# Optimization experiments

Hardware: AMD Instinct MI355X
Metric: run time of the kernel (lower is better)

## Reference

```python
import jax, jax.numpy as jnp
import numpy as np

N_NODES = 100000
N_EDGES = 300000
N_TYPES = 3
HID = 128
EMB = 64
N_GRAPHS = 4096
T_STEPS = 4


def setup_inputs() -> dict:
    key = jax.random.key(0)
    ks = jax.random.split(key, 12)
    s = 1.0 / np.sqrt(HID)
    return {
        "node_features": jax.random.normal(ks[0], (N_NODES, HID), jnp.float32),
        "edge_index": jax.random.randint(ks[1], (N_TYPES, 2, N_EDGES), 0, N_NODES),
        "node_to_graph_id": jnp.sort(jax.random.randint(ks[2], (N_NODES,), 0, N_GRAPHS)),
        "W_msg": jax.random.normal(ks[3], (N_TYPES, HID, HID), jnp.float32) * s,
        "b_msg": jnp.zeros((N_TYPES, HID), jnp.float32),
        "W_ih": jax.random.normal(ks[4], (3 * HID, HID), jnp.float32) * s,
        "W_hh": jax.random.normal(ks[5], (3 * HID, HID), jnp.float32) * s,
        "b_ih": jnp.zeros((3 * HID,), jnp.float32),
        "b_hh": jnp.zeros((3 * HID,), jnp.float32),
        "W_proj": jax.random.normal(ks[6], (EMB, HID), jnp.float32) * s,
        "b_proj": jnp.zeros((EMB,), jnp.float32),
        "W_gate": jax.random.normal(ks[7], (EMB, HID), jnp.float32) * s,
        "b_gate": jnp.zeros((EMB,), jnp.float32),
    }


def _gru_cell(m, h, W_ih, W_hh, b_ih, b_hh):
    # torch.nn.GRUCell math; gates ordered (r, z, n)
    gi = m @ W_ih.T + b_ih          # [N, 3H]
    gh = h @ W_hh.T + b_hh          # [N, 3H]
    i_r, i_z, i_n = jnp.split(gi, 3, axis=-1)
    h_r, h_z, h_n = jnp.split(gh, 3, axis=-1)
    r = jax.nn.sigmoid(i_r + h_r)
    z = jax.nn.sigmoid(i_z + h_z)
    n = jnp.tanh(i_n + r * h_n)
    return (1.0 - z) * n + z * h


def reference(node_features, edge_index, node_to_graph_id,
              W_msg, b_msg, W_ih, W_hh, b_ih, b_hh,
              W_proj, b_proj, W_gate, b_gate):
    h = node_features  # [N, H]

    def per_type(eidx, W, b, h):
        src, dst = eidx[0], eidx[1]
        m = h[src] @ W + b  # gather + per-edge-type linear, [E, H]
        return jax.ops.segment_sum(m, dst, num_segments=N_NODES)

    for _ in range(T_STEPS):  # fixed small T: python loop is fine
        msgs = jax.vmap(per_type, in_axes=(0, 0, 0, None))(edge_index, W_msg, b_msg, h)
        m = msgs.sum(axis=0)  # [N, H] aggregated over edge types
        h = _gru_cell(m, h, W_ih, W_hh, b_ih, b_hh)

    # gated index_add graph readout (mlp_down is identity)
    proj = h @ W_proj.T + b_proj                 # [N, E]
    gate = jax.nn.sigmoid(h @ W_gate.T + b_gate)  # [N, E]
    graph_feats = jax.ops.segment_sum(gate * proj, node_to_graph_id,
                                      num_segments=N_GRAPHS)
    return graph_feats
```

## Files before the change

kernel.cpp:

```cpp
#include <hip/hip_runtime.h>
#include <hip/hip_bf16.h>
#include <math.h>

#define NN 100000
#define NNP 100096
#define NE 300000
#define HID 128
#define EMB 64
#define NG 4096
#define DEG_CAP 32
#define XS 512

typedef __bf16 bf16x8 __attribute__((ext_vector_type(8)));
typedef float  f32x16 __attribute__((ext_vector_type(16)));
typedef short  short8 __attribute__((ext_vector_type(8)));

typedef const __attribute__((address_space(1))) unsigned int* gas_u32;
typedef __attribute__((address_space(3))) unsigned int* las_u32;

__device__ __forceinline__ void gload16(const void* g, void* l) {
    __builtin_amdgcn_global_load_lds((gas_u32)g, (las_u32)l, 16, 0, 0);
}

__device__ __forceinline__ float bf2f(unsigned short u) {
    unsigned int x = ((unsigned int)u) << 16;
    return __builtin_bit_cast(float, x);
}
__device__ __forceinline__ unsigned short f2bf(float f) {
    unsigned int x = __builtin_bit_cast(unsigned int, f);
    unsigned int r = x + 0x7fff + ((x >> 16) & 1);
    return (unsigned short)(r >> 16);
}
__device__ __forceinline__ float sigm(float x) { return 1.f / (1.f + __expf(-x)); }

#define MFMA(A, B, C) __builtin_amdgcn_mfma_f32_32x32x16_bf16( \
    __builtin_bit_cast(bf16x8, A), __builtin_bit_cast(bf16x8, B), C, 0, 0, 0)

__global__ __launch_bounds__(256) void k_init(const float* __restrict__ nf,
                                              unsigned short* __restrict__ Y) {
    int id = blockIdx.x * 256 + threadIdx.x;
    int n = id >> 7, c = id & 127;
    Y[(long)n * HID + c] = (n < NN) ? f2bf(nf[(long)n * HID + c]) : (unsigned short)0;
}

__global__ __launch_bounds__(256) void k_build_csr(const int* __restrict__ ei,
                                                   int* __restrict__ deg,
                                                   int* __restrict__ csr) {
    int id = blockIdx.x * 256 + threadIdx.x;
    if (id >= 3 * NE) return;
    int t = id / NE;
    int i = id - t * NE;
    int src = ei[(t * 2 + 0) * NE + i];
    int dst = ei[(t * 2 + 1) * NE + i];
    int p = atomicAdd(&deg[t * NN + dst], 1);
    if (p < DEG_CAP) csr[((long)t * NN + dst) * DEG_CAP + p] = src;
}

__global__ __launch_bounds__(256) void k_pack_deg(const int* __restrict__ deg,
                                                  int4* __restrict__ degp) {
    int n = blockIdx.x * 256 + threadIdx.x;
    if (n >= NNP) return;
    int4 v; v.x = 0; v.y = 0; v.z = 0; v.w = 0;
    if (n < NN) { v.x = deg[n]; v.y = deg[NN + n]; v.z = deg[2 * NN + n]; }
    degp[n] = v;
}

__global__ __launch_bounds__(512) void k_build_w(const float* __restrict__ Wmsg,
                                                 const float* __restrict__ Wih,
                                                 const float* __restrict__ Whh,
                                                 unsigned short* __restrict__ Bf) {
    int np = blockIdx.x;
    int k = threadIdx.x;
    int c = np >> 2, sec = np & 3;
    float v = 0.f;
    if (k < 384) {
        if (sec < 3) {
            int t = k >> 7, kk = k & 127;
            const float* wm = Wmsg + ((long)t * HID + kk) * HID;
            const float* wi = Wih + (long)(sec * HID + c) * HID;
            float s = 0.f;
            for (int j = 0; j < HID; j++) s += wm[j] * wi[j];
            v = s;
        }
    } else {
        int kk = k - 384;
        if (sec == 0)      v = Whh[(long)c * HID + kk];
        else if (sec == 1) v = Whh[(long)(HID + c) * HID + kk];
        else if (sec == 3) v = Whh[(long)(2 * HID + c) * HID + kk];
    }
    int nb = np >> 5, nl = np & 31;
    int k16 = k >> 4, kgg = (k >> 3) & 1, e = k & 7;
    Bf[((((nb * 32 + k16) * 2 + kgg) * 32 + nl) << 3) + e] = f2bf(v);
}

__global__ __launch_bounds__(512) void k_build_bias(const float* __restrict__ bih,
                                                    const float* __restrict__ bhh,
                                                    const float* __restrict__ bmsg,
                                                    const float* __restrict__ Wih,
                                                    float* __restrict__ bbig,
                                                    float* __restrict__ Bdeg) {
    int np = threadIdx.x;
    int c = np >> 2, sec = np & 3;
    float b;
    if (sec == 0)      b = bih[c] + bhh[c];
    else if (sec == 1) b = bih[HID + c] + bhh[HID + c];
    else if (sec == 2) b = bih[2 * HID + c];
    else               b = bhh[2 * HID + c];
    bbig[np] = b;
    for (int t = 0; t < 3; t++) {
        float s = 0.f;
        if (sec < 3) {
            const float* wi = Wih + (long)(sec * HID + c) * HID;
            const float* bm = bmsg + t * HID;
            for (int j = 0; j < HID; j++) s += bm[j] * wi[j];
        }
        Bdeg[t * 512 + np] = s;
    }
}

__global__ __launch_bounds__(256) void k_agg(const unsigned short* __restrict__ Y,
                                             unsigned short* __restrict__ X,
                                             const int* __restrict__ deg,
                                             const int* __restrict__ csr) {
    const int lane = threadIdx.x & 63;
    const long n = (long)blockIdx.x * 4 + (threadIdx.x >> 6);
    const int g = lane >> 4;
    const int c16 = lane & 15;
    const int l31 = lane & 31;

    int d[3], il[3];
#pragma unroll
    for (int t = 0; t < 3; t++) {
        int dt = deg[t * NN + n];
        d[t] = dt > DEG_CAP ? DEG_CAP : dt;
        il[t] = csr[((long)t * NN + n) * DEG_CAP + l31];
    }
#pragma unroll
    for (int t = 0; t < 3; t++) {
        float acc[8] = {0.f, 0.f, 0.f, 0.f, 0.f, 0.f, 0.f, 0.f};
        int rounds = (d[t] + 3) >> 2;
        for (int r = 0; r < rounds; r++) {
            int j = r * 4 + g;
            int idx = __shfl(il[t], j & 31);
            if (j < d[t]) {
                short8 v = *(const short8*)(Y + (long)idx * HID + c16 * 8);
#pragma unroll
                for (int q = 0; q < 8; q++) acc[q] += bf2f((unsigned short)v[q]);
            }
        }
#pragma unroll
        for (int q = 0; q < 8; q++) {
            acc[q] += __shfl_xor(acc[q], 16);
            acc[q] += __shfl_xor(acc[q], 32);
        }
        if (g == 0) {
            short8 o;
#pragma unroll
            for (int q = 0; q < 8; q++) o[q] = (short)f2bf(acc[q]);
            *(short8*)(X + n * XS + t * HID + c16 * 8) = o;
        }
    }
    if (g == 1) {
        short8 v = *(const short8*)(Y + n * HID + c16 * 8);
        *(short8*)(X + n * XS + 384 + c16 * 8) = v;
    }
}

__global__ __launch_bounds__(512, 4) void k_gru_mfma(
        const unsigned short* __restrict__ X,
        const unsigned short* __restrict__ Y,
        unsigned short* __restrict__ Yw,
        const unsigned short* __restrict__ Bf,
        const float* __restrict__ bbig, const float* __restrict__ Bdeg,
        const int4* __restrict__ degp) {
    __shared__ char lds[66048];

    const int tid = threadIdx.x;
    const int lane = tid & 63;
    const int wv = tid >> 6;
    const int r31 = lane & 31;
    const int kg = lane >> 5;
    const long row0 = (long)blockIdx.x * 64;

    f32x16 acc[2][2];
#pragma unroll
    for (int i = 0; i < 2; i++)
#pragma unroll
        for (int j = 0; j < 2; j++) acc[i][j] = (f32x16)(0.0f);

    const char* pAl = (const char*)X + (row0 + r31) * 1024 + kg * 16;
#define STAGE_A(HALF)                                                           \
    {                                                                           \
        _Pragma("unroll")                                                       \
        for (int jj = 0; jj < 4; jj++) {                                        \
            const int f = wv * 4 + jj;                                          \
            gload16(pAl + (f & 1) * 32768 + ((HALF) * 16 + (f >> 1)) * 32,      \
                    lds + f * 1024);                                            \
        }                                                                       \
    }

    const unsigned short* pB0 = Bf + (wv * 2 + 0) * 16384 + lane * 8;
    const unsigned short* pB1 = Bf + (wv * 2 + 1) * 16384 + lane * 8;

    STAGE_A(0);
    __syncthreads();

#pragma unroll
    for (int k16l = 0; k16l < 16; k16l++) {
        short8 a0 = *(const short8*)(lds + (k16l * 2 + 0) * 1024 + lane * 16);
        short8 a1 = *(const short8*)(lds + (k16l * 2 + 1) * 1024 + lane * 16);
        short8 b0 = *(const short8*)(pB0 + k16l * 512);
        short8 b1 = *(const short8*)(pB1 + k16l * 512);
        acc[0][0] = MFMA(a0, b0, acc[0][0]);
        acc[0][1] = MFMA(a0, b1, acc[0][1]);
        acc[1][0] = MFMA(a1, b0, acc[1][0]);
        acc[1][1] = MFMA(a1, b1, acc[1][1]);
    }

    __syncthreads();
    STAGE_A(1);
    __syncthreads();

#pragma unroll
    for (int k16l = 0; k16l < 16; k16l++) {
        const int k16g = 16 + k16l;
        short8 a0 = *(const short8*)(lds + (k16l * 2 + 0) * 1024 + lane * 16);
        short8 a1 = *(const short8*)(lds + (k16l * 2 + 1) * 1024 + lane * 16);
        short8 b0 = *(const short8*)(pB0 + k16g * 512);
        short8 b1 = *(const short8*)(pB1 + k16g * 512);
        acc[0][0] = MFMA(a0, b0, acc[0][0]);
        acc[0][1] = MFMA(a0, b1, acc[0][1]);
        acc[1][0] = MFMA(a1, b0, acc[1][0]);
        acc[1][1] = MFMA(a1, b1, acc[1][1]);
    }

    float* EX = (float*)lds;
    const int ch = tid & 127;
    const int r5b = tid >> 7;
    const float4 bb = *(const float4*)(bbig + ch * 4);
    const float4 q0v = *(const float4*)(Bdeg + ch * 4);
    const float4 q1v = *(const float4*)(Bdeg + 512 + ch * 4);
    const float4 q2v = *(const float4*)(Bdeg + 1024 + ch * 4);

#pragma unroll
    for (int half = 0; half < 2; half++) {
        __syncthreads();
#pragma unroll
        for (int ct = 0; ct < 2; ct++) {
            const int col = wv * 64 + ct * 32 + r31;
#pragma unroll
            for (int reg = 0; reg < 16; reg++) {
                int r5 = (reg & 3) + 8 * (reg >> 2) + 4 * kg;
                EX[r5 * 516 + col] = half ? acc[1][ct][reg] : acc[0][ct][reg];
            }
        }
        __syncthreads();
#pragma unroll
        for (int i = 0; i < 8; i++) {
            const int r5 = r5b + 4 * i;
            long grow = row0 + half * 32 + r5;
            int4 dg = degp[grow];
            float dgx = (float)dg.x, dgy = (float)dg.y, dgz = (float)dg.z;
            float4 v = *(const float4*)(EX + r5 * 516 + ch * 4);
            float Sr = v.x + bb.x + dgx * q0v.x + dgy * q1v.x + dgz * q2v.x;
            float Sz = v.y + bb.y + dgx * q0v.y + dgy * q1v.y + dgz * q2v.y;
            float In = v.z + bb.z + dgx * q0v.z + dgy * q1v.z + dgz * q2v.z;
            float Hn = v.w + bb.w;
            float rr = sigm(Sr);
            float zz = sigm(Sz);
            float tt = In + rr * Hn;
            float ee = __expf(2.f * tt);
            float nn = 1.f - 2.f / (ee + 1.f);
            float hv = (1.f - zz) * nn + zz * bf2f(Y[grow * HID + ch]);
            Yw[grow * HID + ch] = f2bf(hv);
        }
    }
}

__global__ __launch_bounds__(256) void k_readout(const unsigned short* __restrict__ Y,
                                                 const int* __restrict__ n2g,
                                                 const float* __restrict__ Wp,
                                                 const float* __restrict__ bp,
                                                 const float* __restrict__ Wg,
                                                 const float* __restrict__ bg,
                                                 float* __restrict__ out) {
    __shared__ float hs[32][132];
    __shared__ float Ws[64][129];
    int tid = threadIdx.x;
    long row0 = (long)blockIdx.x * 32;
    int rg = tid >> 5, cg = tid & 31;
    float acc[4][4];
#pragma unroll
    for (int r = 0; r < 4; r++)
#pragma unroll
        for (int c = 0; c < 4; c++) acc[r][c] = 0.f;

#pragma unroll
    for (int p = 0; p < 2; p++) {
        int e = p * 256 + tid;
        int r = e >> 4, c8 = e & 15;
        short8 v = *(const short8*)(Y + (row0 + r) * HID + c8 * 8);
#pragma unroll
        for (int j = 0; j < 8; j++) hs[r][c8 * 8 + j] = bf2f((unsigned short)v[j]);
    }
    for (int kc = 0; kc < 128; kc += 64) {
        __syncthreads();
#pragma unroll
        for (int p = 0; p < 8; p++) {
            int idx = p * 256 + tid;
            int j = idx >> 4, q = idx & 15;
            const float* Wsrc = (j < 64) ? Wp : Wg;
            float4 w = *(const float4*)&Wsrc[(j & 63) * HID + kc + q * 4];
            Ws[q * 4 + 0][j] = w.x;
            Ws[q * 4 + 1][j] = w.y;
            Ws[q * 4 + 2][j] = w.z;
            Ws[q * 4 + 3][j] = w.w;
        }
        __syncthreads();
#pragma unroll 8
        for (int k = 0; k < 64; k++) {
            float a[4], w[4];
#pragma unroll
            for (int r = 0; r < 4; r++) a[r] = hs[rg * 4 + r][kc + k];
#pragma unroll
            for (int c = 0; c < 4; c++) w[c] = Ws[k][cg + 32 * c];
#pragma unroll
            for (int r = 0; r < 4; r++)
#pragma unroll
                for (int c = 0; c < 4; c++) acc[r][c] += a[r] * w[c];
        }
    }
#pragma unroll
    for (int r = 0; r < 4; r++) {
        long row = row0 + rg * 4 + r;
        if (row < NN) {
            int g = n2g[row];
            float pv0 = acc[r][0] + bp[cg];
            float pv1 = acc[r][1] + bp[cg + 32];
            float gv0 = acc[r][2] + bg[cg];
            float gv1 = acc[r][3] + bg[cg + 32];
            atomicAdd(&out[g * EMB + cg],      pv0 * sigm(gv0));
            atomicAdd(&out[g * EMB + cg + 32], pv1 * sigm(gv1));
        }
    }
}

extern "C" void kernel_launch(void* const* d_in, const int* in_sizes, int n_in,
                              void* d_out, int out_size, void* d_ws, size_t ws_size,
                              hipStream_t stream) {
    const float* node_features = (const float*)d_in[0];
    const int*   edge_index    = (const int*)d_in[1];
    const int*   n2g           = (const int*)d_in[2];
    const float* W_msg         = (const float*)d_in[3];
    const float* b_msg         = (const float*)d_in[4];
    const float* W_ih          = (const float*)d_in[5];
    const float* W_hh          = (const float*)d_in[6];
    const float* b_ih          = (const float*)d_in[7];
    const float* b_hh          = (const float*)d_in[8];
    const float* W_proj        = (const float*)d_in[9];
    const float* b_proj        = (const float*)d_in[10];
    const float* W_gate        = (const float*)d_in[11];
    const float* b_gate        = (const float*)d_in[12];

    char* ws = (char*)d_ws;
    unsigned short* X    = (unsigned short*)(ws);
    unsigned short* Y    = (unsigned short*)(ws + 102498304);
    unsigned short* Bf   = (unsigned short*)(ws + 128122880);
    float*          bbig = (float*)         (ws + 128647168);
    float*          Bdeg = (float*)         (ws + 128649216);
    int4*           degp = (int4*)          (ws + 128655360);
    int*            deg  = (int*)           (ws + 130256896);
    int*            csr  = (int*)           (ws + 131456896);

    float* out = (float*)d_out;

    hipMemsetAsync(out, 0, (size_t)NG * EMB * sizeof(float), stream);
    hipMemsetAsync(deg, 0, (size_t)3 * NN * sizeof(int), stream);

    k_init<<<dim3((NNP * HID) / 256), dim3(256), 0, stream>>>(node_features, Y);
    k_build_csr<<<dim3((3 * NE + 255) / 256), dim3(256), 0, stream>>>(edge_index, deg, csr);
    k_pack_deg<<<dim3(NNP / 256), dim3(256), 0, stream>>>(deg, degp);
    k_build_w<<<dim3(512), dim3(512), 0, stream>>>(W_msg, W_ih, W_hh, Bf);
    k_build_bias<<<dim3(1), dim3(512), 0, stream>>>(b_ih, b_hh, b_msg, W_ih, bbig, Bdeg);

    for (int step = 0; step < 4; step++) {
        k_agg<<<dim3(NN / 4), dim3(256), 0, stream>>>(Y, X, deg, csr);
        k_gru_mfma<<<dim3(NNP / 64), dim3(512), 0, stream>>>(X, Y, Y, Bf,
                                                             bbig, Bdeg, degp);
    }
    k_readout<<<dim3(NN / 32), dim3(256), 0, stream>>>(Y, n2g, W_proj, b_proj,
                                                       W_gate, b_gate, out);
}
```

Before: 854.0 us.

## Fuse neighbor aggregation into GRU MFMA kernel with ping-pong hidden buffers

Merges the gather/segment-sum kernel into the GRU MFMA kernel. Each block aggregates neighbor rows for its 64 nodes straight into LDS in the MFMA A-tile layout, so the 512-wide intermediate X buffer is never written to or read from global memory. The hidden state now alternates between two buffers across steps, which avoids read/write races. The cost is lower gather parallelism per node: each 16-lane group walks its edge list serially, and there is one block per 64 rows with the MFMA work waiting behind the gather phase.

```diff
diff --git a/kernel.cpp b/kernel.cpp
--- a/kernel.cpp
+++ b/kernel.cpp
@@ -9,18 +9,10 @@
 #define EMB 64
 #define NG 4096
 #define DEG_CAP 32
-#define XS 512
 
 typedef __bf16 bf16x8 __attribute__((ext_vector_type(8)));
 typedef float  f32x16 __attribute__((ext_vector_type(16)));
 typedef short  short8 __attribute__((ext_vector_type(8)));
-
-typedef const __attribute__((address_space(1))) unsigned int* gas_u32;
-typedef __attribute__((address_space(3))) unsigned int* las_u32;
-
-__device__ __forceinline__ void gload16(const void* g, void* l) {
-    __builtin_amdgcn_global_load_lds((gas_u32)g, (las_u32)l, 16, 0, 0);
-}
 
 __device__ __forceinline__ float bf2f(unsigned short u) {
     unsigned int x = ((unsigned int)u) << 16;
@@ -118,116 +110,73 @@
     }
 }
 
-__global__ __launch_bounds__(256) void k_agg(const unsigned short* __restrict__ Y,
-                                             unsigned short* __restrict__ X,
-                                             const int* __restrict__ deg,
-                                             const int* __restrict__ csr) {
-    const int lane = threadIdx.x & 63;
-    const long n = (long)blockIdx.x * 4 + (threadIdx.x >> 6);
-    const int g = lane >> 4;
-    const int c16 = lane & 15;
-    const int l31 = lane & 31;
-
-    int d[3], il[3];
-#pragma unroll
-    for (int t = 0; t < 3; t++) {
-        int dt = deg[t * NN + n];
-        d[t] = dt > DEG_CAP ? DEG_CAP : dt;
-        il[t] = csr[((long)t * NN + n) * DEG_CAP + l31];
-    }
-#pragma unroll
-    for (int t = 0; t < 3; t++) {
-        float acc[8] = {0.f, 0.f, 0.f, 0.f, 0.f, 0.f, 0.f, 0.f};
-        int rounds = (d[t] + 3) >> 2;
-        for (int r = 0; r < rounds; r++) {
-            int j = r * 4 + g;
-            int idx = __shfl(il[t], j & 31);
-            if (j < d[t]) {
-                short8 v = *(const short8*)(Y + (long)idx * HID + c16 * 8);
-#pragma unroll
-                for (int q = 0; q < 8; q++) acc[q] += bf2f((unsigned short)v[q]);
-            }
-        }
-#pragma unroll
-        for (int q = 0; q < 8; q++) {
-            acc[q] += __shfl_xor(acc[q], 16);
-            acc[q] += __shfl_xor(acc[q], 32);
-        }
-        if (g == 0) {
-            short8 o;
-#pragma unroll
-            for (int q = 0; q < 8; q++) o[q] = (short)f2bf(acc[q]);
-            *(short8*)(X + n * XS + t * HID + c16 * 8) = o;
-        }
-    }
-    if (g == 1) {
-        short8 v = *(const short8*)(Y + n * HID + c16 * 8);
-        *(short8*)(X + n * XS + 384 + c16 * 8) = v;
-    }
-}
-
-__global__ __launch_bounds__(512, 4) void k_gru_mfma(
-        const unsigned short* __restrict__ X,
-        const unsigned short* __restrict__ Y,
-        unsigned short* __restrict__ Yw,
+__global__ __launch_bounds__(512, 4) void k_step(
+        const unsigned short* __restrict__ Yin,
+        unsigned short* __restrict__ Yout,
         const unsigned short* __restrict__ Bf,
         const float* __restrict__ bbig, const float* __restrict__ Bdeg,
-        const int4* __restrict__ degp) {
+        const int4* __restrict__ degp,
+        const int* __restrict__ deg,
+        const int* __restrict__ csr) {
     __shared__ char lds[66048];
 
     const int tid = threadIdx.x;
     const int lane = tid & 63;
     const int wv = tid >> 6;
+    const int sec = lane >> 4;
+    const int c16 = lane & 15;
+    const long row0 = (long)blockIdx.x * 64;
+
+#pragma unroll
+    for (int i = 0; i < 8; i++) {
+        const int rloc = wv * 8 + i;
+        const long n = row0 + rloc;
+        int d = 0, il0 = 0, il1 = 0;
+        if (sec < 3 && n < NN) {
+            d = deg[sec * NN + n];
+            if (d > DEG_CAP) d = DEG_CAP;
+            const long cb = ((long)sec * NN + n) * DEG_CAP;
+            il0 = csr[cb + c16];
+            il1 = csr[cb + 16 + c16];
+        }
+        float ac[8] = {0.f, 0.f, 0.f, 0.f, 0.f, 0.f, 0.f, 0.f};
+#pragma unroll 2
+        for (int j = 0; j < d; j++) {
+            int idx = __shfl((j < 16) ? il0 : il1, (lane & 48) + (j & 15));
+            short8 v = *(const short8*)(Yin + (long)idx * HID + c16 * 8);
+#pragma unroll
+            for (int q = 0; q < 8; q++) ac[q] += bf2f((unsigned short)v[q]);
+        }
+        short8 o;
+        if (sec == 3) {
+            o = *(const short8*)(Yin + n * HID + c16 * 8);
+        } else {
+#pragma unroll
+            for (int q = 0; q < 8; q++) o[q] = (short)f2bf(ac[q]);
+        }
+        const int k16 = sec * 8 + (c16 >> 1);
+        const int f = k16 * 2 + (rloc >> 5);
+        *(short8*)(lds + f * 1024 + (((c16 & 1) << 5) + (rloc & 31)) * 16) = o;
+    }
+
     const int r31 = lane & 31;
-    const int kg = lane >> 5;
-    const long row0 = (long)blockIdx.x * 64;
-
-    f32x16 acc[2][2];
-#pragma unroll
-    for (int i = 0; i < 2; i++)
-#pragma unroll
-        for (int j = 0; j < 2; j++) acc[i][j] = (f32x16)(0.0f);
-
-    const char* pAl = (const char*)X + (row0 + r31) * 1024 + kg * 16;
-#define STAGE_A(HALF)                                                           \
-    {                                                                           \
-        _Pragma("unroll")                                                       \
-        for (int jj = 0; jj < 4; jj++) {                                        \
-            const int f = wv * 4 + jj;                                          \
-            gload16(pAl + (f & 1) * 32768 + ((HALF) * 16 + (f >> 1)) * 32,      \
-                    lds + f * 1024);                                            \
-        }                                                                       \
-    }
-
     const unsigned short* pB0 = Bf + (wv * 2 + 0) * 16384 + lane * 8;
     const unsigned short* pB1 = Bf + (wv * 2 + 1) * 16384 + lane * 8;
 
-    STAGE_A(0);
+    f32x16 acc[2][2];
+#pragma unroll
+    for (int i = 0; i < 2; i++)
+#pragma unroll
+        for (int j = 0; j < 2; j++) acc[i][j] = (f32x16)(0.0f);
+
     __syncthreads();
 
 #pragma unroll
-    for (int k16l = 0; k16l < 16; k16l++) {
-        short8 a0 = *(const short8*)(lds + (k16l * 2 + 0) * 1024 + lane * 16);
-        short8 a1 = *(const short8*)(lds + (k16l * 2 + 1) * 1024 + lane * 16);
-        short8 b0 = *(const short8*)(pB0 + k16l * 512);
-        short8 b1 = *(const short8*)(pB1 + k16l * 512);
-        acc[0][0] = MFMA(a0, b0, acc[0][0]);
-        acc[0][1] = MFMA(a0, b1, acc[0][1]);
-        acc[1][0] = MFMA(a1, b0, acc[1][0]);
-        acc[1][1] = MFMA(a1, b1, acc[1][1]);
-    }
-
-    __syncthreads();
-    STAGE_A(1);
-    __syncthreads();
-
-#pragma unroll
-    for (int k16l = 0; k16l < 16; k16l++) {
-        const int k16g = 16 + k16l;
-        short8 a0 = *(const short8*)(lds + (k16l * 2 + 0) * 1024 + lane * 16);
-        short8 a1 = *(const short8*)(lds + (k16l * 2 + 1) * 1024 + lane * 16);
-        short8 b0 = *(const short8*)(pB0 + k16g * 512);
-        short8 b1 = *(const short8*)(pB1 + k16g * 512);
+    for (int k16 = 0; k16 < 32; k16++) {
+        short8 a0 = *(const short8*)(lds + (k16 * 2 + 0) * 1024 + lane * 16);
+        short8 a1 = *(const short8*)(lds + (k16 * 2 + 1) * 1024 + lane * 16);
+        short8 b0 = *(const short8*)(pB0 + k16 * 512);
+        short8 b1 = *(const short8*)(pB1 + k16 * 512);
         acc[0][0] = MFMA(a0, b0, acc[0][0]);
         acc[0][1] = MFMA(a0, b1, acc[0][1]);
         acc[1][0] = MFMA(a1, b0, acc[1][0]);
@@ -241,6 +190,7 @@
     const float4 q0v = *(const float4*)(Bdeg + ch * 4);
     const float4 q1v = *(const float4*)(Bdeg + 512 + ch * 4);
     const float4 q2v = *(const float4*)(Bdeg + 1024 + ch * 4);
+    const int kg = lane >> 5;
 
 #pragma unroll
     for (int half = 0; half < 2; half++) {
@@ -271,8 +221,8 @@
             float tt = In + rr * Hn;
             float ee = __expf(2.f * tt);
             float nn = 1.f - 2.f / (ee + 1.f);
-            float hv = (1.f - zz) * nn + zz * bf2f(Y[grow * HID + ch]);
-            Yw[grow * HID + ch] = f2bf(hv);
+            float hv = (1.f - zz) * nn + zz * bf2f(Yin[grow * HID + ch]);
+            Yout[grow * HID + ch] = f2bf(hv);
         }
     }
 }
@@ -363,31 +313,31 @@
     const float* b_gate        = (const float*)d_in[12];
 
     char* ws = (char*)d_ws;
-    unsigned short* X    = (unsigned short*)(ws);
-    unsigned short* Y    = (unsigned short*)(ws + 102498304);
-    unsigned short* Bf   = (unsigned short*)(ws + 128122880);
-    float*          bbig = (float*)         (ws + 128647168);
-    float*          Bdeg = (float*)         (ws + 128649216);
-    int4*           degp = (int4*)          (ws + 128655360);
-    int*            deg  = (int*)           (ws + 130256896);
-    int*            csr  = (int*)           (ws + 131456896);
+    unsigned short* Y0   = (unsigned short*)(ws);
+    unsigned short* Y1   = (unsigned short*)(ws + 25624576);
+    unsigned short* Bf   = (unsigned short*)(ws + 51249152);
+    float*          bbig = (float*)         (ws + 51773440);
+    float*          Bdeg = (float*)         (ws + 51775488);
+    int4*           degp = (int4*)          (ws + 51781632);
+    int*            deg  = (int*)           (ws + 53383168);
+    int*            csr  = (int*)           (ws + 54583168);
 
     float* out = (float*)d_out;
 
     hipMemsetAsync(out, 0, (size_t)NG * EMB * sizeof(float), stream);
     hipMemsetAsync(deg, 0, (size_t)3 * NN * sizeof(int), stream);
 
-    k_init<<<dim3((NNP * HID) / 256), dim3(256), 0, stream>>>(node_features, Y);
+    k_init<<<dim3((NNP * HID) / 256), dim3(256), 0, stream>>>(node_features, Y0);
     k_build_csr<<<dim3((3 * NE + 255) / 256), dim3(256), 0, stream>>>(edge_index, deg, csr);
     k_pack_deg<<<dim3(NNP / 256), dim3(256), 0, stream>>>(deg, degp);
     k_build_w<<<dim3(512), dim3(512), 0, stream>>>(W_msg, W_ih, W_hh, Bf);
     k_build_bias<<<dim3(1), dim3(512), 0, stream>>>(b_ih, b_hh, b_msg, W_ih, bbig, Bdeg);
 
-    for (int step = 0; step < 4; step++) {
-        k_agg<<<dim3(NN / 4), dim3(256), 0, stream>>>(Y, X, deg, csr);
-        k_gru_mfma<<<dim3(NNP / 64), dim3(512), 0, stream>>>(X, Y, Y, Bf,
-                                                             bbig, Bdeg, degp);
-    }
-    k_readout<<<dim3(NN / 32), dim3(256), 0, stream>>>(Y, n2g, W_proj, b_proj,
+    k_step<<<dim3(NNP / 64), dim3(512), 0, stream>>>(Y0, Y1, Bf, bbig, Bdeg, degp, deg, csr);
+    k_step<<<dim3(NNP / 64), dim3(512), 0, stream>>>(Y1, Y0, Bf, bbig, Bdeg, degp, deg, csr);
+    k_step<<<dim3(NNP / 64), dim3(512), 0, stream>>>(Y0, Y1, Bf, bbig, Bdeg, degp, deg, csr);
+    k_step<<<dim3(NNP / 64), dim3(512), 0, stream>>>(Y1, Y0, Bf, bbig, Bdeg, degp, deg, csr);
+
+    k_readout<<<dim3(NN / 32), dim3(256), 0, stream>>>(Y0, n2g, W_proj, b_proj,
                                                        W_gate, b_gate, out);
 }
```

Result: slower. 874.1 us (+2.4%).

## Double GRU GEMM row tile, stage all A into LDS, prefetch B

Applied to the files above, without the earlier changes.

The GRU MFMA kernel now handles 128 rows per block instead of 64, with four accumulator row groups, so each B fragment loaded from global memory is reused across twice as many rows. Both K-halves of A are staged into 128 KB of dynamic LDS up front, so the second half loads while the first half computes and the mid-kernel barrier/restage is gone. B fragments are software-prefetched one K-step ahead in registers. The cost is one resident block per CU (launch bounds lowered to 2), more accumulator registers, and a dependence on large dynamic LDS being allowed at launch.

```diff
diff --git a/kernel.cpp b/kernel.cpp
--- a/kernel.cpp
+++ b/kernel.cpp
@@ -166,37 +166,37 @@
     }
 }
 
-__global__ __launch_bounds__(512, 4) void k_gru_mfma(
+__global__ __launch_bounds__(512, 2) void k_gru_mfma(
         const unsigned short* __restrict__ X,
         const unsigned short* __restrict__ Y,
         unsigned short* __restrict__ Yw,
         const unsigned short* __restrict__ Bf,
         const float* __restrict__ bbig, const float* __restrict__ Bdeg,
         const int4* __restrict__ degp) {
-    __shared__ char lds[66048];
+    extern __shared__ char lds[];
 
     const int tid = threadIdx.x;
     const int lane = tid & 63;
     const int wv = tid >> 6;
     const int r31 = lane & 31;
     const int kg = lane >> 5;
-    const long row0 = (long)blockIdx.x * 64;
-
-    f32x16 acc[2][2];
-#pragma unroll
-    for (int i = 0; i < 2; i++)
+    const long row0 = (long)blockIdx.x * 128;
+
+    f32x16 acc[4][2];
+#pragma unroll
+    for (int i = 0; i < 4; i++)
 #pragma unroll
         for (int j = 0; j < 2; j++) acc[i][j] = (f32x16)(0.0f);
 
-    const char* pAl = (const char*)X + (row0 + r31) * 1024 + kg * 16;
-#define STAGE_A(HALF)                                                           \
-    {                                                                           \
-        _Pragma("unroll")                                                       \
-        for (int jj = 0; jj < 4; jj++) {                                        \
-            const int f = wv * 4 + jj;                                          \
-            gload16(pAl + (f & 1) * 32768 + ((HALF) * 16 + (f >> 1)) * 32,      \
-                    lds + f * 1024);                                            \
-        }                                                                       \
+    const char* base = (const char*)X + (row0 + r31) * 1024 + kg * 16;
+#define STAGE_A(H)                                                            \
+    {                                                                         \
+        _Pragma("unroll")                                                     \
+        for (int jj = 0; jj < 8; jj++) {                                      \
+            const int f = wv * 8 + jj;                                        \
+            gload16(base + (long)(f & 3) * 32768 + ((H) * 16 + (f >> 2)) * 32,\
+                    lds + ((H) * 64 + f) * 1024);                             \
+        }                                                                     \
     }
 
     const unsigned short* pB0 = Bf + (wv * 2 + 0) * 16384 + lane * 8;
@@ -204,46 +204,69 @@
 
     STAGE_A(0);
     __syncthreads();
-
-#pragma unroll
-    for (int k16l = 0; k16l < 16; k16l++) {
-        short8 a0 = *(const short8*)(lds + (k16l * 2 + 0) * 1024 + lane * 16);
-        short8 a1 = *(const short8*)(lds + (k16l * 2 + 1) * 1024 + lane * 16);
-        short8 b0 = *(const short8*)(pB0 + k16l * 512);
-        short8 b1 = *(const short8*)(pB1 + k16l * 512);
-        acc[0][0] = MFMA(a0, b0, acc[0][0]);
-        acc[0][1] = MFMA(a0, b1, acc[0][1]);
-        acc[1][0] = MFMA(a1, b0, acc[1][0]);
-        acc[1][1] = MFMA(a1, b1, acc[1][1]);
-    }
-
+    STAGE_A(1);
+#undef STAGE_A
+
+    short8 pe0 = *(const short8*)(pB0);
+    short8 pe1 = *(const short8*)(pB1);
+    short8 po0 = *(const short8*)(pB0 + 512);
+    short8 po1 = *(const short8*)(pB1 + 512);
+
+#define KSTEP(K16, B0, B1)                                                    \
+    {                                                                         \
+        const char* fb = lds + (((K16) >> 4) * 64 + ((K16) & 15) * 4) * 1024  \
+                         + lane * 16;                                         \
+        short8 a0 = *(const short8*)(fb);                                     \
+        short8 a1 = *(const short8*)(fb + 1024);                              \
+        short8 a2 = *(const short8*)(fb + 2048);                              \
+        short8 a3 = *(const short8*)(fb + 3072);                              \
+        acc[0][0] = MFMA(a0, B0, acc[0][0]);                                  \
+        acc[0][1] = MFMA(a0, B1, acc[0][1]);                                  \
+        acc[1][0] = MFMA(a1, B0, acc[1][0]);                                  \
+        acc[1][1] = MFMA(a1, B1, acc[1][1]);                                  \
+        acc[2][0] = MFMA(a2, B0, acc[2][0]);                                  \
+        acc[2][1] = MFMA(a2, B1, acc[2][1]);                                  \
+        acc[3][0] = MFMA(a3, B0, acc[3][0]);                                  \
+        acc[3][1] = MFMA(a3, B1, acc[3][1]);                                  \
+    }
+
+#pragma unroll
+    for (int it = 0; it < 8; it++) {
+        const int k0 = 2 * it;
+        KSTEP(k0, pe0, pe1);
+        pe0 = *(const short8*)(pB0 + (k0 + 2) * 512);
+        pe1 = *(const short8*)(pB1 + (k0 + 2) * 512);
+        KSTEP(k0 + 1, po0, po1);
+        po0 = *(const short8*)(pB0 + (k0 + 3) * 512);
+        po1 = *(const short8*)(pB1 + (k0 + 3) * 512);
+    }
     __syncthreads();
-    STAGE_A(1);
-    __syncthreads();
-
-#pragma unroll
-    for (int k16l = 0; k16l < 16; k16l++) {
-        const int k16g = 16 + k16l;
-        short8 a0 = *(const short8*)(lds + (k16l * 2 + 0) * 1024 + lane * 16);
-        short8 a1 = *(const short8*)(lds + (k16l * 2 + 1) * 1024 + lane * 16);
-        short8 b0 = *(const short8*)(pB0 + k16g * 512);
-        short8 b1 = *(const short8*)(pB1 + k16g * 512);
-        acc[0][0] = MFMA(a0, b0, acc[0][0]);
-        acc[0][1] = MFMA(a0, b1, acc[0][1]);
-        acc[1][0] = MFMA(a1, b0, acc[1][0]);
-        acc[1][1] = MFMA(a1, b1, acc[1][1]);
-    }
+#pragma unroll
+    for (int it = 8; it < 16; it++) {
+        const int k0 = 2 * it;
+        KSTEP(k0, pe0, pe1);
+        if (it < 15) {
+            pe0 = *(const short8*)(pB0 + (k0 + 2) * 512);
+            pe1 = *(const short8*)(pB1 + (k0 + 2) * 512);
+        }
+        KSTEP(k0 + 1, po0, po1);
+        if (it < 15) {
+            po0 = *(const short8*)(pB0 + (k0 + 3) * 512);
+            po1 = *(const short8*)(pB1 + (k0 + 3) * 512);
+        }
+    }
+#undef KSTEP
 
     float* EX = (float*)lds;
     const int ch = tid & 127;
     const int r5b = tid >> 7;
-    const float4 bb = *(const float4*)(bbig + ch * 4);
+    const float4 bb  = *(const float4*)(bbig + ch * 4);
     const float4 q0v = *(const float4*)(Bdeg + ch * 4);
     const float4 q1v = *(const float4*)(Bdeg + 512 + ch * 4);
     const float4 q2v = *(const float4*)(Bdeg + 1024 + ch * 4);
 
 #pragma unroll
-    for (int half = 0; half < 2; half++) {
+    for (int q = 0; q < 4; q++) {
         __syncthreads();
 #pragma unroll
         for (int ct = 0; ct < 2; ct++) {
@@ -251,14 +274,14 @@
 #pragma unroll
             for (int reg = 0; reg < 16; reg++) {
                 int r5 = (reg & 3) + 8 * (reg >> 2) + 4 * kg;
-                EX[r5 * 516 + col] = half ? acc[1][ct][reg] : acc[0][ct][reg];
+                EX[r5 * 516 + col] = acc[q][ct][reg];
             }
         }
         __syncthreads();
 #pragma unroll
         for (int i = 0; i < 8; i++) {
             const int r5 = r5b + 4 * i;
-            long grow = row0 + half * 32 + r5;
+            long grow = row0 + q * 32 + r5;
             int4 dg = degp[grow];
             float dgx = (float)dg.x, dgy = (float)dg.y, dgz = (float)dg.z;
             float4 v = *(const float4*)(EX + r5 * 516 + ch * 4);
@@ -385,8 +408,8 @@
 
     for (int step = 0; step < 4; step++) {
         k_agg<<<dim3(NN / 4), dim3(256), 0, stream>>>(Y, X, deg, csr);
-        k_gru_mfma<<<dim3(NNP / 64), dim3(512), 0, stream>>>(X, Y, Y, Bf,
-                                                             bbig, Bdeg, degp);
+        k_gru_mfma<<<dim3(NNP / 128), dim3(512), 131072, stream>>>(X, Y, Y, Bf,
+                                                                   bbig, Bdeg, degp);
     }
     k_readout<<<dim3(NN / 32), dim3(256), 0, stream>>>(Y, n2g, W_proj, b_proj,
                                                        W_gate, b_gate, out);
```

New measurement: 953.9 us. 1.12x slower.

## Retile GRU MFMA kernel into 128x256 blocks with double-buffered LDS staging

Applied to the files above, without the earlier changes.

The GRU GEMM now uses a 2D grid. Each block computes 128 rows by 256 output columns, with the 8 waves laid out 2x4. Both the A tile and the B weight tile are streamed into LDS through global_load_lds in 16 k-steps, using a ping-pong double buffer so the next stage loads while the current one computes. Previously each block did all columns for 64 rows and read B directly from global memory. The epilogue is split into 16-row chunks with a smaller LDS footprint. The intent is to raise weight reuse and hide load latency, at the cost of more barriers and each block reading the A rows twice.

```diff
diff --git a/kernel.cpp b/kernel.cpp
--- a/kernel.cpp
+++ b/kernel.cpp
@@ -173,14 +173,17 @@
         const unsigned short* __restrict__ Bf,
         const float* __restrict__ bbig, const float* __restrict__ Bdeg,
         const int4* __restrict__ degp) {
-    __shared__ char lds[66048];
+    __shared__ char lds[49152];
 
     const int tid = threadIdx.x;
     const int lane = tid & 63;
     const int wv = tid >> 6;
+    const int wr = wv >> 2;
+    const int wc = wv & 3;
     const int r31 = lane & 31;
     const int kg = lane >> 5;
-    const long row0 = (long)blockIdx.x * 64;
+    const int bn = blockIdx.x;
+    const long row0 = (long)blockIdx.y * 128;
 
     f32x16 acc[2][2];
 #pragma unroll
@@ -188,91 +191,87 @@
 #pragma unroll
         for (int j = 0; j < 2; j++) acc[i][j] = (f32x16)(0.0f);
 
-    const char* pAl = (const char*)X + (row0 + r31) * 1024 + kg * 16;
-#define STAGE_A(HALF)                                                           \
-    {                                                                           \
-        _Pragma("unroll")                                                       \
-        for (int jj = 0; jj < 4; jj++) {                                        \
-            const int f = wv * 4 + jj;                                          \
-            gload16(pAl + (f & 1) * 32768 + ((HALF) * 16 + (f >> 1)) * 32,      \
-                    lds + f * 1024);                                            \
-        }                                                                       \
-    }
-
-    const unsigned short* pB0 = Bf + (wv * 2 + 0) * 16384 + lane * 8;
-    const unsigned short* pB1 = Bf + (wv * 2 + 1) * 16384 + lane * 8;
-
-    STAGE_A(0);
-    __syncthreads();
-
-#pragma unroll
-    for (int k16l = 0; k16l < 16; k16l++) {
-        short8 a0 = *(const short8*)(lds + (k16l * 2 + 0) * 1024 + lane * 16);
-        short8 a1 = *(const short8*)(lds + (k16l * 2 + 1) * 1024 + lane * 16);
-        short8 b0 = *(const short8*)(pB0 + k16l * 512);
-        short8 b1 = *(const short8*)(pB1 + k16l * 512);
-        acc[0][0] = MFMA(a0, b0, acc[0][0]);
-        acc[0][1] = MFMA(a0, b1, acc[0][1]);
-        acc[1][0] = MFMA(a1, b0, acc[1][0]);
-        acc[1][1] = MFMA(a1, b1, acc[1][1]);
-    }
-
-    __syncthreads();
-    STAGE_A(1);
-    __syncthreads();
-
-#pragma unroll
-    for (int k16l = 0; k16l < 16; k16l++) {
-        const int k16g = 16 + k16l;
-        short8 a0 = *(const short8*)(lds + (k16l * 2 + 0) * 1024 + lane * 16);
-        short8 a1 = *(const short8*)(lds + (k16l * 2 + 1) * 1024 + lane * 16);
-        short8 b0 = *(const short8*)(pB0 + k16g * 512);
-        short8 b1 = *(const short8*)(pB1 + k16g * 512);
-        acc[0][0] = MFMA(a0, b0, acc[0][0]);
-        acc[0][1] = MFMA(a0, b1, acc[0][1]);
-        acc[1][0] = MFMA(a1, b0, acc[1][0]);
-        acc[1][1] = MFMA(a1, b1, acc[1][1]);
-    }
+    const char* pAsrc = (const char*)X + (row0 + (wv & 3) * 32 + r31) * 1024
+                        + (wv >> 2) * 32 + kg * 16;
+    const char* pBsrc = (const char*)Bf + ((long)(bn * 8 + wv) * 32) * 1024
+                        + lane * 16;
+
+#define STAGE(BUFOFF, KS)                                                     \
+    {                                                                         \
+        gload16(pAsrc + (KS) * 64, lds + (BUFOFF) + wv * 1024);               \
+        gload16(pBsrc + ((long)(KS) * 2 + 0) * 1024,                          \
+                lds + (BUFOFF) + 8192 + (0 * 8 + wv) * 1024);                 \
+        gload16(pBsrc + ((long)(KS) * 2 + 1) * 1024,                          \
+                lds + (BUFOFF) + 8192 + (1 * 8 + wv) * 1024);                 \
+    }
+
+    STAGE(0, 0);
+
+#pragma unroll
+    for (int ks = 0; ks < 16; ks++) {
+        const int cur = (ks & 1) * 24576;
+        __syncthreads();
+        if (ks < 15) STAGE(24576 - cur, ks + 1);
+        const char* Ab = lds + cur;
+        const char* Bb = lds + cur + 8192;
+#pragma unroll
+        for (int k16l = 0; k16l < 2; k16l++) {
+            short8 a0 = *(const short8*)(Ab + (k16l * 4 + wr * 2 + 0) * 1024 + lane * 16);
+            short8 a1 = *(const short8*)(Ab + (k16l * 4 + wr * 2 + 1) * 1024 + lane * 16);
+            short8 b0 = *(const short8*)(Bb + (k16l * 8 + wc * 2 + 0) * 1024 + lane * 16);
+            short8 b1 = *(const short8*)(Bb + (k16l * 8 + wc * 2 + 1) * 1024 + lane * 16);
+            acc[0][0] = MFMA(a0, b0, acc[0][0]);
+            acc[0][1] = MFMA(a0, b1, acc[0][1]);
+            acc[1][0] = MFMA(a1, b0, acc[1][0]);
+            acc[1][1] = MFMA(a1, b1, acc[1][1]);
+        }
+    }
+#undef STAGE
 
     float* EX = (float*)lds;
-    const int ch = tid & 127;
-    const int r5b = tid >> 7;
-    const float4 bb = *(const float4*)(bbig + ch * 4);
-    const float4 q0v = *(const float4*)(Bdeg + ch * 4);
-    const float4 q1v = *(const float4*)(Bdeg + 512 + ch * 4);
-    const float4 q2v = *(const float4*)(Bdeg + 1024 + ch * 4);
-
-#pragma unroll
-    for (int half = 0; half < 2; half++) {
-        __syncthreads();
-#pragma unroll
-        for (int ct = 0; ct < 2; ct++) {
-            const int col = wv * 64 + ct * 32 + r31;
-#pragma unroll
-            for (int reg = 0; reg < 16; reg++) {
-                int r5 = (reg & 3) + 8 * (reg >> 2) + 4 * kg;
-                EX[r5 * 516 + col] = half ? acc[1][ct][reg] : acc[0][ct][reg];
+#pragma unroll
+    for (int c = 0; c < 8; c++) {
+        __syncthreads();
+        if (wr == (c >> 2)) {
+            const int mt = (c >> 1) & 1;
+            const int q8 = (c & 1) * 8;
+#pragma unroll
+            for (int ct = 0; ct < 2; ct++) {
+                const int col = wc * 64 + ct * 32 + r31;
+#pragma unroll
+                for (int rr = 0; rr < 8; rr++) {
+                    int rwl = (rr & 3) + 8 * (rr >> 2) + 4 * kg;
+                    EX[rwl * 264 + col] = acc[mt][ct][q8 + rr];
+                }
             }
         }
         __syncthreads();
-#pragma unroll
-        for (int i = 0; i < 8; i++) {
-            const int r5 = r5b + 4 * i;
-            long grow = row0 + half * 32 + r5;
+        {
+            const int row16 = tid >> 5;
+            const long grow = row0 + c * 16 + row16;
             int4 dg = degp[grow];
             float dgx = (float)dg.x, dgy = (float)dg.y, dgz = (float)dg.z;
-            float4 v = *(const float4*)(EX + r5 * 516 + ch * 4);
-            float Sr = v.x + bb.x + dgx * q0v.x + dgy * q1v.x + dgz * q2v.x;
-            float Sz = v.y + bb.y + dgx * q0v.y + dgy * q1v.y + dgz * q2v.y;
-            float In = v.z + bb.z + dgx * q0v.z + dgy * q1v.z + dgz * q2v.z;
-            float Hn = v.w + bb.w;
-            float rr = sigm(Sr);
-            float zz = sigm(Sz);
-            float tt = In + rr * Hn;
-            float ee = __expf(2.f * tt);
-            float nn = 1.f - 2.f / (ee + 1.f);
-            float hv = (1.f - zz) * nn + zz * bf2f(Y[grow * HID + ch]);
-            Yw[grow * HID + ch] = f2bf(hv);
+#pragma unroll
+            for (int i = 0; i < 2; i++) {
+                const int chl = (tid & 31) + i * 32;
+                const int gch = bn * 64 + chl;
+                float4 v  = *(const float4*)(EX + row16 * 264 + chl * 4);
+                float4 bb = *(const float4*)(bbig + bn * 256 + chl * 4);
+                float4 q0 = *(const float4*)(Bdeg + bn * 256 + chl * 4);
+                float4 q1 = *(const float4*)(Bdeg + 512 + bn * 256 + chl * 4);
+                float4 q2 = *(const float4*)(Bdeg + 1024 + bn * 256 + chl * 4);
+                float Sr = v.x + bb.x + dgx * q0.x + dgy * q1.x + dgz * q2.x;
+                float Sz = v.y + bb.y + dgx * q0.y + dgy * q1.y + dgz * q2.y;
+                float In = v.z + bb.z + dgx * q0.z + dgy * q1.z + dgz * q2.z;
+                float Hn = v.w + bb.w;
+                float rr = sigm(Sr);
+                float zz = sigm(Sz);
+                float tt = In + rr * Hn;
+                float ee = __expf(2.f * tt);
+                float nn = 1.f - 2.f / (ee + 1.f);
+                float hv = (1.f - zz) * nn + zz * bf2f(Y[grow * HID + gch]);
+                Yw[grow * HID + gch] = f2bf(hv);
+            }
         }
     }
 }
@@ -385,8 +384,8 @@
 
     for (int step = 0; step < 4; step++) {
         k_agg<<<dim3(NN / 4), dim3(256), 0, stream>>>(Y, X, deg, csr);
-        k_gru_mfma<<<dim3(NNP / 64), dim3(512), 0, stream>>>(X, Y, Y, Bf,
-                                                             bbig, Bdeg, degp);
+        k_gru_mfma<<<dim3(2, NNP / 128), dim3(512), 0, stream>>>(X, Y, Y, Bf,
+                                                                 bbig, Bdeg, degp);
     }
     k_readout<<<dim3(NN / 32), dim3(256), 0, stream>>>(Y, n2g, W_proj, b_proj,
                                                        W_gate, b_gate, out);
```

After: 878.0 us. 1.03x slower.
